# Kernel tuning notes

Hardware: AMD Instinct MI355X
Metric: run time of the kernel (lower is better)

Reference implementation:

```python
import jax, jax.numpy as jnp
import numpy as np

N = 50000   # nodes
E = 800000  # edges (before self loops)
G = 8       # graphs in batch
IN, H, HD = 3, 64, 128


def setup_inputs() -> dict:
    key = jax.random.key(0)
    ks = jax.random.split(key, 12)
    s = 0.1  # weight scale
    return {
        "x": jax.random.normal(ks[0], (N, IN), jnp.float32),
        "edge_index": jax.random.randint(ks[1], (2, E), 0, N, dtype=jnp.int32),
        "batch": jnp.sort(jax.random.randint(ks[2], (N,), 0, G, dtype=jnp.int32)),
        "W1": s * jax.random.normal(ks[3], (IN, H), jnp.float32),
        "a_src1": s * jax.random.normal(ks[4], (H,), jnp.float32),
        "a_dst1": s * jax.random.normal(ks[5], (H,), jnp.float32),
        "b1": jnp.zeros((H,), jnp.float32),
        "W2": s * jax.random.normal(ks[6], (H, H), jnp.float32),
        "a_src2": s * jax.random.normal(ks[7], (H,), jnp.float32),
        "a_dst2": s * jax.random.normal(ks[8], (H,), jnp.float32),
        "b2": jnp.zeros((H,), jnp.float32),
        "Wh1": s * jax.random.normal(ks[9], (H, HD), jnp.float32),
        "bh1": jnp.zeros((HD,), jnp.float32),
        "Wh2": s * jax.random.normal(ks[10], (HD, 1), jnp.float32),
        "bh2": jnp.zeros((1,), jnp.float32),
    }


def gat_conv(x, src, dst, W, a_src, a_dst, b, n_nodes):
    """Single-head GATConv (PyG defaults: slope 0.2, self-loops, bias)."""
    h = x @ W                           # [N, H]
    e_s = h @ a_src                     # [N] per-node source logits
    e_d = h @ a_dst                     # [N] per-node target logits
    e = jax.nn.leaky_relu(e_s[src] + e_d[dst], 0.2)  # [E']
    # segment softmax over incoming edges of each target node
    m = jax.ops.segment_max(e, dst, num_segments=n_nodes)
    ex = jnp.exp(e - m[dst])
    denom = jax.ops.segment_sum(ex, dst, num_segments=n_nodes)
    alpha = ex / denom[dst]             # [E']
    out = jax.ops.segment_sum(h[src] * alpha[:, None], dst, num_segments=n_nodes)
    return out + b


def reference(x, edge_index, batch, W1, a_src1, a_dst1, b1,
              W2, a_src2, a_dst2, b2, Wh1, bh1, Wh2, bh2):
    n = x.shape[0]
    loops = jnp.arange(n, dtype=edge_index.dtype)
    src = jnp.concatenate([edge_index[0], loops])  # add self loops
    dst = jnp.concatenate([edge_index[1], loops])

    h = jax.nn.relu(gat_conv(x, src, dst, W1, a_src1, a_dst1, b1, n))
    h = jax.nn.relu(gat_conv(h, src, dst, W2, a_src2, a_dst2, b2, n))

    # global mean pool per graph
    sums = jax.ops.segment_sum(h, batch, num_segments=G)          # [G, H]
    cnt = jax.ops.segment_sum(jnp.ones((n,), h.dtype), batch, num_segments=G)
    pooled = sums / jnp.maximum(cnt, 1.0)[:, None]

    # value head: Linear -> ReLU -> Linear
    return jax.nn.relu(pooled @ Wh1 + bh1) @ Wh2 + bh2            # [G, 1]
```

## Files before the change

kernel.cpp:

```cpp
#include <hip/hip_runtime.h>
#include <math.h>

#define NN 50000
#define NE 800000
#define NG 8
#define H 64
#define HD 128
#define CAP 48
#define NCHUNK (CAP / 4)
#define NSLICE 64
#define EPT 8
#define ETH (NE / EPT)
#define ECHUNKS ((ETH + 255) / 256)
#define NODEB ((NN * H) / 256)
#define NPB 1536
#define GB 2048
#define GSTRIDE (GB * 4)
#define NBUCK 200
#define BNODES 250
#define RCAP 4800
#define LCAP 32

typedef unsigned short ushort_t;
typedef _Float16 half_t;
typedef _Float16 half2_t __attribute__((ext_vector_type(2)));
typedef int int4v __attribute__((ext_vector_type(4)));

__global__ void k_binA(const int* __restrict__ src, const int* __restrict__ dst,
                       unsigned* __restrict__ cursor, unsigned* __restrict__ recs,
                       const float* __restrict__ x, const float* __restrict__ W,
                       const float* __restrict__ asrc, const float* __restrict__ adst,
                       const float* __restrict__ W2, half2_t* __restrict__ W2p,
                       half_t* __restrict__ h, float* __restrict__ es, float* __restrict__ ed) {
    int bid = blockIdx.x;
    if (bid < ECHUNKS) {
        __shared__ unsigned lcnt[NBUCK];
        __shared__ unsigned lbuf[NBUCK][LCAP];
        for (int i = threadIdx.x; i < NBUCK; i += 256) lcnt[i] = 0;
        __syncthreads();
        int t = bid * 256 + threadIdx.x;
        int e0 = t * EPT;
        if (e0 < NE) {
            int4v da = *(const int4v*)(dst + e0);
            int4v db = *(const int4v*)(dst + e0 + 4);
            int4v sa = *(const int4v*)(src + e0);
            int4v sb = *(const int4v*)(src + e0 + 4);
            int ds[8] = {da.x, da.y, da.z, da.w, db.x, db.y, db.z, db.w};
            int ss[8] = {sa.x, sa.y, sa.z, sa.w, sb.x, sb.y, sb.z, sb.w};
            #pragma unroll
            for (int i = 0; i < 8; ++i) {
                unsigned d = (unsigned)ds[i];
                unsigned bk = d / BNODES;
                unsigned dloc = d - bk * BNODES;
                unsigned rec = ((unsigned)ss[i] << 8) | dloc;
                unsigned l = atomicAdd(&lcnt[bk], 1u);
                if (l < LCAP) lbuf[bk][l] = rec;
                else {
                    unsigned g = atomicAdd(&cursor[bk], 1u);
                    if (g < RCAP) recs[(size_t)bk * RCAP + g] = rec;
                }
            }
        }
        __syncthreads();
        for (int b = threadIdx.x; b < NBUCK; b += 256) {
            unsigned c = lcnt[b]; c = c > LCAP ? LCAP : c;
            if (c) {
                unsigned base = atomicAdd(&cursor[b], c);
                for (unsigned i = 0; i < c; ++i)
                    if (base + i < RCAP) recs[(size_t)b * RCAP + base + i] = lbuf[b][i];
            }
        }
    } else if (bid < ECHUNKS + NPB) {
        for (int nb = bid - ECHUNKS; nb < NODEB; nb += NPB) {
            int nid = nb * 256 + threadIdx.x;
            int node = nid >> 6, lane = nid & 63;
            if (node < NN) {
                float x0 = x[node*3+0], x1 = x[node*3+1], x2 = x[node*3+2];
                float hv = x0*W[lane] + x1*W[64+lane] + x2*W[128+lane];
                __builtin_nontemporal_store((half_t)hv, h + (size_t)node*64 + lane);
                float s = hv * asrc[lane], d = hv * adst[lane];
                #pragma unroll
                for (int o = 32; o > 0; o >>= 1) { s += __shfl_xor(s, o); d += __shfl_xor(d, o); }
                if (lane == 0) { es[node] = s; ed[node] = d; }
            }
        }
    } else {
        for (int i = threadIdx.x; i < (H/2) * 64; i += 256) {
            int k2 = i >> 6, ln = i & 63;
            half2_t v;
            v.x = (_Float16)W2[(2*k2)*64 + ln];
            v.y = (_Float16)W2[(2*k2+1)*64 + ln];
            W2p[i] = v;
        }
    }
}

__global__ void k_buildB(const unsigned* __restrict__ cursor, const unsigned* __restrict__ recs,
                         ushort_t* __restrict__ csr, int* __restrict__ deg) {
    __shared__ unsigned lcnt[BNODES];
    __shared__ ushort_t lcsr[BNODES * CAP];
    int b = blockIdx.x;
    for (int i = threadIdx.x; i < BNODES; i += 256) lcnt[i] = 0;
    __syncthreads();
    unsigned total = cursor[b]; if (total > RCAP) total = RCAP;
    for (unsigned i = threadIdx.x; i < total; i += 256) {
        unsigned rec = recs[(size_t)b * RCAP + i];
        unsigned dloc = rec & 255u;
        unsigned srcv = rec >> 8;
        unsigned slot = atomicAdd(&lcnt[dloc], 1u);
        if (slot < CAP) lcsr[dloc * CAP + slot] = (ushort_t)srcv;
    }
    __syncthreads();
    const unsigned* ls = (const unsigned*)lcsr;
    unsigned* gc = (unsigned*)(csr + (size_t)b * BNODES * CAP);
    for (int i = threadIdx.x; i < BNODES * CAP / 2; i += 256) gc[i] = ls[i];
    for (int d = threadIdx.x; d < BNODES; d += 256) {
        unsigned c = lcnt[d];
        deg[b * BNODES + d] = c > CAP ? CAP : (int)c;
    }
}

#define GPREFETCH(node_nx)                                                       \
    int nN = 0, s0N = 0; float hsN = 0.f, ednN = 0.f, esnN = 0.f;                \
    if ((node_nx) < NN) {                                                        \
        nN   = deg[node_nx];                                                     \
        hsN  = (float)hH[(size_t)(node_nx)*64 + lane];                           \
        ednN = ed[node_nx]; esnN = es[node_nx];                                  \
        s0N  = csr[(size_t)(node_nx) * CAP + lane];                              \
    }

#define GPROLOGUE(node0)                                                         \
    int nC = 0, s0C = 0; float hsC = 0.f, ednC = 0.f, esnC = 0.f;                \
    if ((node0) < NN) {                                                          \
        nC   = deg[node0]; nC = nC > CAP ? CAP : nC;                             \
        hsC  = (float)hH[(size_t)(node0)*64 + lane];                             \
        ednC = ed[node0]; esnC = es[node0];                                      \
        s0C  = csr[(size_t)(node0) * CAP + lane];                                \
    }

#define GROTATE                                                                  \
    nC = nN > CAP ? CAP : nN; s0C = s0N; hsC = hsN; ednC = ednN; esnC = esnN;

#define GATHER_BODY                                                              \
    float e0 = es[s0C] + ednC;                                                   \
    e0 = e0 > 0.f ? e0 : 0.2f * e0;                                              \
    float p0 = (lane < nC) ? __expf(e0) : 0.f;                                   \
    float evs = esnC + ednC; evs = evs > 0.f ? evs : 0.2f * evs;                 \
    float ps = __expf(evs);                                                      \
    sidx[lane] = s0C; sp[lane] = p0;                                             \
    int sub = lane >> 4;                                                         \
    int c4  = (lane & 15) * 4;                                                   \
    float4 acc[4];                                                               \
    acc[0] = {0,0,0,0}; acc[1] = {0,0,0,0}; acc[2] = {0,0,0,0}; acc[3] = {0,0,0,0}; \
    float dq = 0.f;                                                              \
    _Pragma("unroll")                                                            \
    for (int c = 0; c < NCHUNK; ++c) {                                           \
        int r = c * 4 + sub;                                                     \
        float q = (r < nC) ? sp[r] : 0.f;                                        \
        int idx = (r < nC) ? sidx[r] : 0;                                        \
        float2 raw = *(const float2*)(hH + (size_t)idx * 64 + c4);               \
        union { float2 f; half_t hh[4]; } u; u.f = raw;                          \
        acc[c & 3].x += (float)u.hh[0] * q;                                      \
        acc[c & 3].y += (float)u.hh[1] * q;                                      \
        acc[c & 3].z += (float)u.hh[2] * q;                                      \
        acc[c & 3].w += (float)u.hh[3] * q;                                      \
        dq += q;                                                                 \
    }                                                                            \
    float4 A;                                                                    \
    A.x = acc[0].x + acc[1].x + acc[2].x + acc[3].x;                             \
    A.y = acc[0].y + acc[1].y + acc[2].y + acc[3].y;                             \
    A.z = acc[0].z + acc[1].z + acc[2].z + acc[3].z;                             \
    A.w = acc[0].w + acc[1].w + acc[2].w + acc[3].w;                             \
    _Pragma("unroll")                                                            \
    for (int o = 16; o <= 32; o <<= 1) {                                         \
        A.x += __shfl_xor(A.x, o); A.y += __shfl_xor(A.y, o);                    \
        A.z += __shfl_xor(A.z, o); A.w += __shfl_xor(A.w, o);                    \
        dq  += __shfl_xor(dq, o);                                                \
    }                                                                            \
    float inv = 1.0f / (dq + ps);                                                \
    float chs;                                                                   \
    {                                                                            \
        int srcl = lane >> 2;                                                    \
        float v0 = __shfl(A.x, srcl);                                            \
        float v1 = __shfl(A.y, srcl);                                            \
        float v2 = __shfl(A.z, srcl);                                            \
        float v3 = __shfl(A.w, srcl);                                            \
        int j = lane & 3;                                                        \
        chs = (j == 0) ? v0 : (j == 1) ? v1 : (j == 2) ? v2 : v3;                \
    }                                                                            \
    float f = fmaxf((chs + ps * hsC) * inv + bl, 0.f);

__global__ void k_gather1(const int* __restrict__ deg, const ushort_t* __restrict__ csr,
                          const float* __restrict__ es, const float* __restrict__ ed,
                          const half_t* __restrict__ hH, const float* __restrict__ b,
                          const half2_t* __restrict__ W2p, const float* __restrict__ as2,
                          const float* __restrict__ ad2,
                          half_t* __restrict__ h2, float* __restrict__ es2,
                          float* __restrict__ ed2) {
    __shared__ int     s_idx[4][64];
    __shared__ float   s_p[4][64];
    __shared__ half2_t s_fh[4][32];
    int lane = threadIdx.x & 63, w = threadIdx.x >> 6;
    int*   sidx = s_idx[w];
    float* sp   = s_p[w];
    float bl = b[lane], as2l = as2[lane], ad2l = ad2[lane];

    int node0 = blockIdx.x * 4 + w;
    GPROLOGUE(node0)
    for (int node = node0; node < NN; node += GSTRIDE) {
        GPREFETCH(node + GSTRIDE)
        GATHER_BODY

        ((half_t*)s_fh[w])[lane] = (half_t)f;
        float hv = 0.f;
        #pragma unroll
        for (int k2 = 0; k2 < 32; ++k2) {
            half2_t w2v = W2p[k2*64 + lane];
            half2_t f2  = s_fh[w][k2];
#if __has_builtin(__builtin_amdgcn_fdot2)
            hv = __builtin_amdgcn_fdot2(f2, w2v, hv, false);
#else
            hv += (float)f2.x * (float)w2v.x + (float)f2.y * (float)w2v.y;
#endif
        }
        h2[(size_t)node*64 + lane] = (half_t)hv;
        float ss = hv * as2l, dd = hv * ad2l;
        #pragma unroll
        for (int o = 32; o > 0; o >>= 1) {
            ss += __shfl_xor(ss, o); dd += __shfl_xor(dd, o);
        }
        if (lane == 0) { es2[node] = ss; ed2[node] = dd; }
        GROTATE
    }
}

__global__ void k_gather2(const int* __restrict__ deg, const ushort_t* __restrict__ csr,
                          const float* __restrict__ es, const float* __restrict__ ed,
                          const half_t* __restrict__ hH, const float* __restrict__ b,
                          const int* __restrict__ batch,
                          float* __restrict__ sums, float* __restrict__ cnt) {
    __shared__ int   s_idx[4][64];
    __shared__ float s_p[4][64];
    __shared__ float part[NG * H];
    __shared__ float pc[NG];
    for (int i = threadIdx.x; i < NG * H; i += 256) part[i] = 0.f;
    if (threadIdx.x < NG) pc[threadIdx.x] = 0.f;
    __syncthreads();

    int lane = threadIdx.x & 63, w = threadIdx.x >> 6;
    int*   sidx = s_idx[w];
    float* sp   = s_p[w];
    float bl = b[lane];

    int node0 = blockIdx.x * 4 + w;
    GPROLOGUE(node0)
    for (int node = node0; node < NN; node += GSTRIDE) {
        GPREFETCH(node + GSTRIDE)
        GATHER_BODY

        int g = batch[node];
        atomicAdd(&part[g * H + lane], f);
        if (lane == 0) atomicAdd(&pc[g], 1.f);
        GROTATE
    }
    __syncthreads();
    int slice = blockIdx.x & (NSLICE - 1);
    float* ssum = sums + (size_t)slice * (NG * H);
    float* scnt = cnt + (size_t)slice * NG;
    for (int i = threadIdx.x; i < NG * H; i += 256) atomicAdd(&ssum[i], part[i]);
    if (threadIdx.x < NG) atomicAdd(&scnt[threadIdx.x], pc[threadIdx.x]);
}

__global__ void k_head(const float* __restrict__ sums, const float* __restrict__ cnt,
                       const float* __restrict__ Wh1, const float* __restrict__ bh1,
                       const float* __restrict__ Wh2, const float* __restrict__ bh2,
                       float* __restrict__ out) {
    __shared__ float pooled[NG * H];
    __shared__ float hidden[NG * HD];
    __shared__ float c_s[NG];
    int t = threadIdx.x;
    if (t < NG) {
        float c = 0.f;
        for (int s = 0; s < NSLICE; ++s) c += cnt[s * NG + t];
        c_s[t] = fmaxf(c, 1.f);
    }
    __syncthreads();
    for (int i = t; i < NG * H; i += blockDim.x) {
        float v = 0.f;
        for (int s = 0; s < NSLICE; ++s) v += sums[(size_t)s * (NG * H) + i];
        pooled[i] = v / c_s[i >> 6];
    }
    __syncthreads();
    for (int i = t; i < NG * HD; i += blockDim.x) {
        int g = i / HD, hd = i % HD;
        float acc = bh1[hd];
        for (int c = 0; c < H; ++c) acc += pooled[g * H + c] * Wh1[c * HD + hd];
        hidden[i] = fmaxf(acc, 0.f);
    }
    __syncthreads();
    if (t < NG) {
        float acc = bh2[0];
        for (int hd = 0; hd < HD; ++hd) acc += hidden[t * HD + hd] * Wh2[hd];
        out[t] = acc;
    }
}

extern "C" void kernel_launch(void* const* d_in, const int* in_sizes, int n_in,
                              void* d_out, int out_size, void* d_ws, size_t ws_size,
                              hipStream_t stream) {
    const float* x    = (const float*)d_in[0];
    const int*   ei   = (const int*)d_in[1];
    const int*   batch= (const int*)d_in[2];
    const float* W1   = (const float*)d_in[3];
    const float* as1  = (const float*)d_in[4];
    const float* ad1  = (const float*)d_in[5];
    const float* b1   = (const float*)d_in[6];
    const float* W2   = (const float*)d_in[7];
    const float* as2  = (const float*)d_in[8];
    const float* ad2  = (const float*)d_in[9];
    const float* b2   = (const float*)d_in[10];
    const float* Wh1  = (const float*)d_in[11];
    const float* bh1  = (const float*)d_in[12];
    const float* Wh2  = (const float*)d_in[13];
    const float* bh2  = (const float*)d_in[14];
    const int* src = ei;
    const int* dst = ei + NE;

    float* ws   = (float*)d_ws;
    half_t* h1  = (half_t*)ws;
    half_t* h2  = (half_t*)(ws + (size_t)NN*32);
    float* es1  = ws + (size_t)NN*64;
    float* ed1  = es1 + NN;
    float* es2  = ed1 + NN;
    float* ed2  = es2 + NN;
    unsigned* cursor = (unsigned*)(ed2 + NN);
    float* sums = (float*)(cursor + NBUCK);
    float* cnt  = sums + (size_t)NSLICE*NG*H;
    int*   deg  = (int*)(cnt + NSLICE*NG);
    ushort_t* csr = (ushort_t*)(deg + NN);
    half2_t* W2p  = (half2_t*)(csr + (size_t)NN*CAP);
    unsigned* recs = (unsigned*)(W2p + (H/2)*64);

    size_t zeroBytes = (size_t)NBUCK*4 + (size_t)NSLICE*NG*H*4 + (size_t)NSLICE*NG*4;

    dim3 blk(256);
    int aBlocks = ECHUNKS + NPB + 1;

    (void)hipMemsetAsync(cursor, 0, zeroBytes, stream);
    k_binA<<<aBlocks, blk, 0, stream>>>(src, dst, cursor, recs, x, W1, as1, ad1,
                                        W2, W2p, h1, es1, ed1);
    k_buildB<<<NBUCK, blk, 0, stream>>>(cursor, recs, csr, deg);
    k_gather1<<<GB, blk, 0, stream>>>(deg, csr, es1, ed1, h1, b1, W2p, as2, ad2,
                                      h2, es2, ed2);
    k_gather2<<<GB, blk, 0, stream>>>(deg, csr, es2, ed2, h2, b2, batch, sums, cnt);
    k_head<<<1, 256, 0, stream>>>(sums, cnt, Wh1, bh1, Wh2, bh2, (float*)d_out);
}
```

Baseline: 131.0 us.

## Move layer-1 projection into CSR build kernel, prefetch source logits, skip empty chunks

```diff
diff --git a/kernel.cpp b/kernel.cpp
--- a/kernel.cpp
+++ b/kernel.cpp
@@ -7,7 +7,6 @@
 #define H 64
 #define HD 128
 #define CAP 48
-#define NCHUNK (CAP / 4)
 #define NSLICE 64
 #define EPT 8
 #define ETH (NE / EPT)
@@ -27,51 +26,77 @@
 typedef int int4v __attribute__((ext_vector_type(4)));
 
 __global__ void k_binA(const int* __restrict__ src, const int* __restrict__ dst,
-                       unsigned* __restrict__ cursor, unsigned* __restrict__ recs,
-                       const float* __restrict__ x, const float* __restrict__ W,
-                       const float* __restrict__ asrc, const float* __restrict__ adst,
-                       const float* __restrict__ W2, half2_t* __restrict__ W2p,
-                       half_t* __restrict__ h, float* __restrict__ es, float* __restrict__ ed) {
+                       unsigned* __restrict__ cursor, unsigned* __restrict__ recs) {
+    __shared__ unsigned lcnt[NBUCK];
+    __shared__ unsigned lbuf[NBUCK][LCAP];
     int bid = blockIdx.x;
-    if (bid < ECHUNKS) {
-        __shared__ unsigned lcnt[NBUCK];
-        __shared__ unsigned lbuf[NBUCK][LCAP];
-        for (int i = threadIdx.x; i < NBUCK; i += 256) lcnt[i] = 0;
+    for (int i = threadIdx.x; i < NBUCK; i += 256) lcnt[i] = 0;
+    __syncthreads();
+    int t = bid * 256 + threadIdx.x;
+    int e0 = t * EPT;
+    if (e0 < NE) {
+        int4v da = *(const int4v*)(dst + e0);
+        int4v db = *(const int4v*)(dst + e0 + 4);
+        int4v sa = *(const int4v*)(src + e0);
+        int4v sb = *(const int4v*)(src + e0 + 4);
+        int ds[8] = {da.x, da.y, da.z, da.w, db.x, db.y, db.z, db.w};
+        int ss[8] = {sa.x, sa.y, sa.z, sa.w, sb.x, sb.y, sb.z, sb.w};
+        #pragma unroll
+        for (int i = 0; i < 8; ++i) {
+            unsigned d = (unsigned)ds[i];
+            unsigned bk = d / BNODES;
+            unsigned dloc = d - bk * BNODES;
+            unsigned rec = ((unsigned)ss[i] << 8) | dloc;
+            unsigned l = atomicAdd(&lcnt[bk], 1u);
+            if (l < LCAP) lbuf[bk][l] = rec;
+            else {
+                unsigned g = atomicAdd(&cursor[bk], 1u);
+                if (g < RCAP) recs[(size_t)bk * RCAP + g] = rec;
+            }
+        }
+    }
+    __syncthreads();
+    for (int b = threadIdx.x; b < NBUCK; b += 256) {
+        unsigned c = lcnt[b]; c = c > LCAP ? LCAP : c;
+        if (c) {
+            unsigned base = atomicAdd(&cursor[b], c);
+            for (unsigned i = 0; i < c; ++i)
+                if (base + i < RCAP) recs[(size_t)b * RCAP + base + i] = lbuf[b][i];
+        }
+    }
+}
+
+__global__ void k_buildB(const unsigned* __restrict__ cursor, const unsigned* __restrict__ recs,
+                         ushort_t* __restrict__ csr, int* __restrict__ deg,
+                         const float* __restrict__ x, const float* __restrict__ W,
+                         const float* __restrict__ asrc, const float* __restrict__ adst,
+                         const float* __restrict__ W2, half2_t* __restrict__ W2p,
+                         half_t* __restrict__ h, float* __restrict__ es, float* __restrict__ ed) {
+    __shared__ unsigned lcnt[BNODES];
+    __shared__ ushort_t lcsr[BNODES * CAP];
+    int bid = blockIdx.x;
+    if (bid < NBUCK) {
+        int b = bid;
+        for (int i = threadIdx.x; i < BNODES; i += 256) lcnt[i] = 0;
         __syncthreads();
-        int t = bid * 256 + threadIdx.x;
-        int e0 = t * EPT;
-        if (e0 < NE) {
-            int4v da = *(const int4v*)(dst + e0);
-            int4v db = *(const int4v*)(dst + e0 + 4);
-            int4v sa = *(const int4v*)(src + e0);
-            int4v sb = *(const int4v*)(src + e0 + 4);
-            int ds[8] = {da.x, da.y, da.z, da.w, db.x, db.y, db.z, db.w};
-            int ss[8] = {sa.x, sa.y, sa.z, sa.w, sb.x, sb.y, sb.z, sb.w};
-            #pragma unroll
-            for (int i = 0; i < 8; ++i) {
-                unsigned d = (unsigned)ds[i];
-                unsigned bk = d / BNODES;
-                unsigned dloc = d - bk * BNODES;
-                unsigned rec = ((unsigned)ss[i] << 8) | dloc;
-                unsigned l = atomicAdd(&lcnt[bk], 1u);
-                if (l < LCAP) lbuf[bk][l] = rec;
-                else {
-                    unsigned g = atomicAdd(&cursor[bk], 1u);
-                    if (g < RCAP) recs[(size_t)bk * RCAP + g] = rec;
-                }
-            }
+        unsigned total = cursor[b]; if (total > RCAP) total = RCAP;
+        for (unsigned i = threadIdx.x; i < total; i += 256) {
+            unsigned rec = recs[(size_t)b * RCAP + i];
+            unsigned dloc = rec & 255u;
+            unsigned srcv = rec >> 8;
+            unsigned slot = atomicAdd(&lcnt[dloc], 1u);
+            if (slot < CAP) lcsr[dloc * CAP + slot] = (ushort_t)srcv;
         }
         __syncthreads();
-        for (int b = threadIdx.x; b < NBUCK; b += 256) {
-            unsigned c = lcnt[b]; c = c > LCAP ? LCAP : c;
-            if (c) {
-                unsigned base = atomicAdd(&cursor[b], c);
-                for (unsigned i = 0; i < c; ++i)
-                    if (base + i < RCAP) recs[(size_t)b * RCAP + base + i] = lbuf[b][i];
-            }
-        }
-    } else if (bid < ECHUNKS + NPB) {
-        for (int nb = bid - ECHUNKS; nb < NODEB; nb += NPB) {
+        const unsigned* ls = (const unsigned*)lcsr;
+        unsigned* gc = (unsigned*)(csr + (size_t)b * BNODES * CAP);
+        for (int i = threadIdx.x; i < BNODES * CAP / 2; i += 256) gc[i] = ls[i];
+        for (int d = threadIdx.x; d < BNODES; d += 256) {
+            unsigned c = lcnt[d];
+            deg[b * BNODES + d] = c > CAP ? CAP : (int)c;
+        }
+    } else if (bid < NBUCK + NPB) {
+        for (int nb = bid - NBUCK; nb < NODEB; nb += NPB) {
             int nid = nb * 256 + threadIdx.x;
             int node = nid >> 6, lane = nid & 63;
             if (node < NN) {
@@ -95,54 +120,46 @@
     }
 }
 
-__global__ void k_buildB(const unsigned* __restrict__ cursor, const unsigned* __restrict__ recs,
-                         ushort_t* __restrict__ csr, int* __restrict__ deg) {
-    __shared__ unsigned lcnt[BNODES];
-    __shared__ ushort_t lcsr[BNODES * CAP];
-    int b = blockIdx.x;
-    for (int i = threadIdx.x; i < BNODES; i += 256) lcnt[i] = 0;
-    __syncthreads();
-    unsigned total = cursor[b]; if (total > RCAP) total = RCAP;
-    for (unsigned i = threadIdx.x; i < total; i += 256) {
-        unsigned rec = recs[(size_t)b * RCAP + i];
-        unsigned dloc = rec & 255u;
-        unsigned srcv = rec >> 8;
-        unsigned slot = atomicAdd(&lcnt[dloc], 1u);
-        if (slot < CAP) lcsr[dloc * CAP + slot] = (ushort_t)srcv;
-    }
-    __syncthreads();
-    const unsigned* ls = (const unsigned*)lcsr;
-    unsigned* gc = (unsigned*)(csr + (size_t)b * BNODES * CAP);
-    for (int i = threadIdx.x; i < BNODES * CAP / 2; i += 256) gc[i] = ls[i];
-    for (int d = threadIdx.x; d < BNODES; d += 256) {
-        unsigned c = lcnt[d];
-        deg[b * BNODES + d] = c > CAP ? CAP : (int)c;
-    }
-}
-
 #define GPREFETCH(node_nx)                                                       \
-    int nN = 0, s0N = 0; float hsN = 0.f, ednN = 0.f, esnN = 0.f;                \
+    int nN = 0, s0N = 0; float hsN = 0.f, ednN = 0.f, esnN = 0.f, esgN = 0.f;    \
     if ((node_nx) < NN) {                                                        \
         nN   = deg[node_nx];                                                     \
         hsN  = (float)hH[(size_t)(node_nx)*64 + lane];                           \
         ednN = ed[node_nx]; esnN = es[node_nx];                                  \
         s0N  = csr[(size_t)(node_nx) * CAP + lane];                              \
+        esgN = es[s0N];                                                          \
     }
 
 #define GPROLOGUE(node0)                                                         \
-    int nC = 0, s0C = 0; float hsC = 0.f, ednC = 0.f, esnC = 0.f;                \
+    int nC = 0, s0C = 0; float hsC = 0.f, ednC = 0.f, esnC = 0.f, esgC = 0.f;    \
     if ((node0) < NN) {                                                          \
         nC   = deg[node0]; nC = nC > CAP ? CAP : nC;                             \
         hsC  = (float)hH[(size_t)(node0)*64 + lane];                             \
         ednC = ed[node0]; esnC = es[node0];                                      \
         s0C  = csr[(size_t)(node0) * CAP + lane];                                \
+        esgC = es[s0C];                                                          \
     }
 
 #define GROTATE                                                                  \
-    nC = nN > CAP ? CAP : nN; s0C = s0N; hsC = hsN; ednC = ednN; esnC = esnN;
+    nC = nN > CAP ? CAP : nN; s0C = s0N; hsC = hsN; ednC = ednN; esnC = esnN;    \
+    esgC = esgN;
+
+#define CHUNK1(c)                                                                \
+    {                                                                            \
+        int r = (c) * 4 + sub;                                                   \
+        float q = (r < nC) ? sp[r] : 0.f;                                        \
+        int idx = (r < nC) ? sidx[r] : 0;                                        \
+        float2 raw = *(const float2*)(hH + (size_t)idx * 64 + c4);               \
+        union { float2 f; half_t hh[4]; } u; u.f = raw;                          \
+        acc[(c) & 3].x += (float)u.hh[0] * q;                                    \
+        acc[(c) & 3].y += (float)u.hh[1] * q;                                    \
+        acc[(c) & 3].z += (float)u.hh[2] * q;                                    \
+        acc[(c) & 3].w += (float)u.hh[3] * q;                                    \
+        dq += q;                                                                 \
+    }
 
 #define GATHER_BODY                                                              \
-    float e0 = es[s0C] + ednC;                                                   \
+    float e0 = esgC + ednC;                                                      \
     e0 = e0 > 0.f ? e0 : 0.2f * e0;                                              \
     float p0 = (lane < nC) ? __expf(e0) : 0.f;                                   \
     float evs = esnC + ednC; evs = evs > 0.f ? evs : 0.2f * evs;                 \
@@ -153,18 +170,9 @@
     float4 acc[4];                                                               \
     acc[0] = {0,0,0,0}; acc[1] = {0,0,0,0}; acc[2] = {0,0,0,0}; acc[3] = {0,0,0,0}; \
     float dq = 0.f;                                                              \
-    _Pragma("unroll")                                                            \
-    for (int c = 0; c < NCHUNK; ++c) {                                           \
-        int r = c * 4 + sub;                                                     \
-        float q = (r < nC) ? sp[r] : 0.f;                                        \
-        int idx = (r < nC) ? sidx[r] : 0;                                        \
-        float2 raw = *(const float2*)(hH + (size_t)idx * 64 + c4);               \
-        union { float2 f; half_t hh[4]; } u; u.f = raw;                          \
-        acc[c & 3].x += (float)u.hh[0] * q;                                      \
-        acc[c & 3].y += (float)u.hh[1] * q;                                      \
-        acc[c & 3].z += (float)u.hh[2] * q;                                      \
-        acc[c & 3].w += (float)u.hh[3] * q;                                      \
-        dq += q;                                                                 \
+    CHUNK1(0) CHUNK1(1) CHUNK1(2) CHUNK1(3) CHUNK1(4) CHUNK1(5)                  \
+    if (nC > 24) {                                                               \
+        CHUNK1(6) CHUNK1(7) CHUNK1(8) CHUNK1(9) CHUNK1(10) CHUNK1(11)            \
     }                                                                            \
     float4 A;                                                                    \
     A.x = acc[0].x + acc[1].x + acc[2].x + acc[3].x;                             \
@@ -344,12 +352,12 @@
     size_t zeroBytes = (size_t)NBUCK*4 + (size_t)NSLICE*NG*H*4 + (size_t)NSLICE*NG*4;
 
     dim3 blk(256);
-    int aBlocks = ECHUNKS + NPB + 1;
+    int bBlocks = NBUCK + NPB + 1;
 
     (void)hipMemsetAsync(cursor, 0, zeroBytes, stream);
-    k_binA<<<aBlocks, blk, 0, stream>>>(src, dst, cursor, recs, x, W1, as1, ad1,
-                                        W2, W2p, h1, es1, ed1);
-    k_buildB<<<NBUCK, blk, 0, stream>>>(cursor, recs, csr, deg);
+    k_binA<<<ECHUNKS, blk, 0, stream>>>(src, dst, cursor, recs);
+    k_buildB<<<bBlocks, blk, 0, stream>>>(cursor, recs, csr, deg,
+                                          x, W1, as1, ad1, W2, W2p, h1, es1, ed1);
     k_gather1<<<GB, blk, 0, stream>>>(deg, csr, es1, ed1, h1, b1, W2p, as2, ad2,
                                       h2, es2, ed2);
     k_gather2<<<GB, blk, 0, stream>>>(deg, csr, es2, ed2, h2, b2, batch, sums, cnt);
```

Measured after the change: 125.5 us. 1.04x faster.
